# Kernel optimization log

Measured on AMD Instinct MI355X. Metric: run time of the kernel, lower is better.

Reference implementation:

```python
import jax, jax.numpy as jnp
import numpy as np

N, E, HIN, H, FC, C, G = 50000, 1600000, 7, 128, 256, 2, 512

def _glorot(k, shape):
    fan = shape[0] + shape[1]
    return jax.random.uniform(k, shape, jnp.float32, -1.0, 1.0) * jnp.sqrt(6.0 / fan)

def setup_inputs() -> dict:
    key = jax.random.key(0)
    ks = jax.random.split(key, 40)
    inp = {}
    inp['x'] = jax.random.normal(ks[0], (N, HIN), jnp.float32)
    inp['edge_index'] = jax.random.randint(ks[1], (2, E), 0, N)
    inp['batch'] = jnp.sort(jax.random.randint(ks[2], (N,), 0, G))
    dims = [(HIN, H), (H, H), (H, H)]
    for i, (di, do) in enumerate(dims):
        kk = jax.random.split(ks[3 + i], 3)
        inp[f'Wl{i}'] = _glorot(kk[0], (di, do))
        inp[f'bl{i}'] = jnp.zeros((do,), jnp.float32)
        inp[f'Wr{i}'] = _glorot(kk[1], (di, do))
        inp[f'br{i}'] = jnp.zeros((do,), jnp.float32)
        inp[f'att{i}'] = _glorot(kk[2], (1, do))[0]  # GATv2 att vector [H]
        inp[f'bo{i}'] = jnp.zeros((do,), jnp.float32)
    inp['fc1_W'] = _glorot(ks[10], (H, FC))
    inp['fc1_b'] = jnp.zeros((FC,), jnp.float32)
    inp['fc2_W'] = _glorot(ks[11], (FC, C))
    inp['fc2_b'] = jnp.zeros((C,), jnp.float32)
    return inp

def reference(x, edge_index, batch,
              Wl0, bl0, Wr0, br0, att0, bo0,
              Wl1, bl1, Wr1, br1, att1, bo1,
              Wl2, bl2, Wr2, br2, att2, bo2,
              fc1_W, fc1_b, fc2_W, fc2_b):
    n = x.shape[0]
    loop = jnp.arange(n)
    src = jnp.concatenate([edge_index[0], loop])  # self-loops (PyG default)
    dst = jnp.concatenate([edge_index[1], loop])

    def conv(h, Wl, bl, Wr, br, att, bo):
        xl = h @ Wl + bl               # [N,H] source transform
        xr = h @ Wr + br               # [N,H] target transform
        m = jax.nn.leaky_relu(xl[src] + xr[dst], 0.2)  # [E+N,H]
        e = m @ att                    # [E+N] attention logits
        emax = jax.ops.segment_max(e, dst, num_segments=n)
        w = jnp.exp(e - emax[dst])
        denom = jax.ops.segment_sum(w, dst, num_segments=n)
        alpha = w / denom[dst]         # per-target softmax
        return jax.ops.segment_sum(alpha[:, None] * xl[src], dst, num_segments=n) + bo

    h = jax.nn.elu(conv(x, Wl0, bl0, Wr0, br0, att0, bo0))
    h = jax.nn.elu(conv(h, Wl1, bl1, Wr1, br1, att1, bo1))
    h = jax.nn.elu(conv(h, Wl2, bl2, Wr2, br2, att2, bo2))

    # global_mean_pool
    sums = jax.ops.segment_sum(h, batch, num_segments=G)
    cnt = jax.ops.segment_sum(jnp.ones((n,), h.dtype), batch, num_segments=G)
    g = sums / jnp.maximum(cnt, 1.0)[:, None]

    z = jax.nn.relu(g @ fc1_W + fc1_b)
    logits = z @ fc2_W + fc2_b
    return jax.nn.log_softmax(logits, axis=1)
```

## Files before the change

kernel.cpp:

```cpp
#include <hip/hip_runtime.h>
#include <hip/hip_fp16.h>
#include <math.h>

#define H 128
#define FCD 256
#define BUKSH 7
#define MAXBUK 512

typedef _Float16 half8 __attribute__((ext_vector_type(8)));
typedef float floatx4 __attribute__((ext_vector_type(4)));
typedef float fv2 __attribute__((ext_vector_type(2)));

__device__ __forceinline__ fv2 h2fv2(__half2 h){
  float2 t = __half22float2(h);
  fv2 r; r.x = t.x; r.y = t.y; return r;
}

template<int CTRL>
__device__ __forceinline__ float dppadd(float x){
  return x + __int_as_float(__builtin_amdgcn_update_dpp(
      0, __float_as_int(x), CTRL, 0xf, 0xf, true));
}
__device__ __forceinline__ float grp16_sum(float x){
  x = dppadd<0x128>(x);
  x = dppadd<0x124>(x);
  x = dppadd<0x122>(x);
  x = dppadd<0x121>(x);
  return x;
}

__global__ __launch_bounds__(256) void k_setup(
    const float* __restrict__ x,
    const float* __restrict__ Wl0, const float* __restrict__ bl0,
    const float* __restrict__ Wr0, const float* __restrict__ br0,
    __half* __restrict__ xl, __half* __restrict__ xr, int n,
    const float* __restrict__ Wl1, const float* __restrict__ Wr1,
    const float* __restrict__ Wl2, const float* __restrict__ Wr2,
    _Float16* __restrict__ Wt,
    const int* __restrict__ ei, int E, int Et, int* __restrict__ bhistM,
    int NB7, int NEB){
  __shared__ int lh[MAXBUK];
  int b = blockIdx.x, t = threadIdx.x;
  if (b < NB7){
    int col = t & 127;
    int n0 = b*16 + (t >> 7)*8;
    float accl[8], accr[8];
    float bL = bl0[col], bR = br0[col];
    #pragma unroll
    for (int q=0;q<8;q++){ accl[q]=bL; accr[q]=bR; }
    #pragma unroll
    for (int k=0;k<7;k++){
      float wl = Wl0[k*H + col];
      float wr = Wr0[k*H + col];
      #pragma unroll
      for (int q=0;q<8;q++){
        int node = n0+q; if (node >= n) node = n-1;
        float hv = x[(size_t)node*7 + k];
        accl[q] = fmaf(hv, wl, accl[q]);
        accr[q] = fmaf(hv, wr, accr[q]);
      }
    }
    #pragma unroll
    for (int q=0;q<8;q++){
      int node = n0+q;
      if (node < n){
        xl[(size_t)node*H + col] = __float2half(accl[q]);
        xr[(size_t)node*H + col] = __float2half(accr[q]);
      }
    }
  } else if (b < NB7 + 256){
    int idx = (b - NB7)*256 + t;
    int e    = idx & 7;
    int lane = (idx >> 3) & 63;
    int kb   = (idx >> 9) & 3;
    int nt   = (idx >> 11) & 15;
    int L    = idx >> 15;
    int m16 = lane & 15, quad = lane >> 4;
    int k = kb*32 + quad*8 + e;
    int nn = nt*16 + m16;
    const float* W = (L==0) ? (nn<H?Wl1:Wr1) : (nn<H?Wl2:Wr2);
    Wt[idx] = (_Float16)W[k*H + (nn&127)];
  } else {
    int r = b - NB7 - 256;
    lh[t] = 0; lh[t+256] = 0;
    __syncthreads();
    int j0 = r*8192;
    #pragma unroll 4
    for (int i=0;i<32;i++){
      int j = j0 + i*256 + t;
      if (j < Et){
        int dst = (j < E) ? ei[E+j] : (j - E);
        atomicAdd(&lh[dst>>BUKSH], 1);
      }
    }
    __syncthreads();
    bhistM[r*MAXBUK + t]       = lh[t];
    bhistM[r*MAXBUK + 256 + t] = lh[t+256];
  }
}

__global__ void k_scanB(const int* __restrict__ bhistM, int nrows,
                        int* __restrict__ bbase, int* __restrict__ bnext){
  int t = threadIdx.x, lane = t & 63, w = t >> 6;
  int v = 0;
  for (int r=0; r<nrows; r++) v += bhistM[r*MAXBUK + t];
  int x = v;
  #pragma unroll
  for (int off=1; off<64; off<<=1){
    int y = __shfl_up(x, off);
    if (lane >= off) x += y;
  }
  __shared__ int ws[8];
  if (lane==63) ws[w] = x;
  __syncthreads();
  int wo = 0;
  #pragma unroll
  for (int i=0;i<8;i++) if (i<w) wo += ws[i];
  int excl = wo + x - v;
  bbase[t] = excl; bnext[t] = excl;
  if (t==511) bbase[512] = wo + x;
}

__global__ void k_bscatter(const int* __restrict__ ei, int E, int Et, int nbuk,
                           int* __restrict__ bnext, unsigned* __restrict__ ebuf){
  __shared__ int lh[MAXBUK];
  __shared__ int lbase[MAXBUK];
  int t = threadIdx.x;
  lh[t] = 0;
  __syncthreads();
  int j0 = blockIdx.x*8192;
  unsigned pk[16]; int bk[16]; int rk[16];
  #pragma unroll
  for (int i=0;i<16;i++){
    int j = j0 + i*512 + t;
    if (j < Et){
      int src, dst;
      if (j < E){ src = ei[j]; dst = ei[E+j]; } else { src = dst = j - E; }
      pk[i] = (unsigned)src | ((unsigned)dst << 16);
      bk[i] = dst >> BUKSH;
      rk[i] = atomicAdd(&lh[bk[i]], 1);
    }
  }
  __syncthreads();
  if (t < nbuk){
    int c = lh[t];
    lbase[t] = c ? atomicAdd(&bnext[t], c) : 0;
  }
  __syncthreads();
  #pragma unroll
  for (int i=0;i<16;i++){
    int j = j0 + i*512 + t;
    if (j < Et) ebuf[lbase[bk[i]] + rk[i]] = pk[i];
  }
}

__global__ void k_bfill(const unsigned* __restrict__ ebuf, const int* __restrict__ bbase,
                        int N, int Et,
                        int* __restrict__ row_ptr, int* __restrict__ csr,
                        int* __restrict__ perm){
  __shared__ int cnt[1<<BUKSH];
  __shared__ int lnxt[1<<BUKSH];
  __shared__ int bh[256];
  __shared__ int sbase[256];
  __shared__ int rk[256];
  __shared__ int ws0[1];
  __shared__ int ws2[4];
  int b = blockIdx.x, t = threadIdx.x;
  if (t < (1<<BUKSH)) cnt[t] = 0;
  bh[t] = 0; rk[t] = 0;
  if (b==0 && t==0) row_ptr[N] = Et;
  __syncthreads();
  int lo = bbase[b], hi = bbase[b+1];
  for (int j = lo + t; j < hi; j += 256){
    unsigned d = ebuf[j] >> 16;
    atomicAdd(&cnt[d & ((1<<BUKSH)-1)], 1);
  }
  __syncthreads();
  int lane = t & 63;
  int mydeg = (t < (1<<BUKSH)) ? cnt[t] : 0;
  int x = mydeg;
  #pragma unroll
  for (int off=1; off<64; off<<=1){
    int y = __shfl_up(x, off);
    if (lane >= off) x += y;
  }
  if (t==63) ws0[0] = x;
  __syncthreads();
  if (t >= 64 && t < 128) x += ws0[0];
  int node = (b<<BUKSH) + t;
  if (t < (1<<BUKSH)){
    int excl = lo + x - mydeg;
    lnxt[t] = excl;
    if (node < N){
      row_ptr[node] = excl;
      atomicAdd(&bh[min(mydeg,255)], 1);
    }
  }
  __syncthreads();
  for (int j = lo + t; j < hi; j += 256){
    unsigned e = ebuf[j];
    int d = (e >> 16) & ((1<<BUKSH)-1);
    int r = atomicAdd(&lnxt[d], 1);
    csr[r] = (int)((e & 0xffff) << 8);
  }
  int bv = bh[t];
  int bx = bv;
  int w2 = t >> 6;
  #pragma unroll
  for (int off=1; off<64; off<<=1){
    int y = __shfl_up(bx, off);
    if (lane >= off) bx += y;
  }
  if (lane==63) ws2[w2] = bx;
  __syncthreads();
  int wo = (w2>0?ws2[0]:0) + (w2>1?ws2[1]:0) + (w2>2?ws2[2]:0);
  sbase[t] = wo + bx - bv;
  __syncthreads();
  if (t < (1<<BUKSH) && node < N){
    int d = min(mydeg,255);
    int r = atomicAdd(&rk[d], 1);
    perm[(b<<BUKSH) + sbase[d] + r] = node;
  }
}

__global__ __launch_bounds__(256) void k_gemm2h(
    const __half* __restrict__ h, const _Float16* __restrict__ Wt,
    const float* __restrict__ bl, const float* __restrict__ br,
    __half* __restrict__ xl, __half* __restrict__ xr, int n){
  int wave = threadIdx.x >> 6, lane = threadIdx.x & 63;
  int m16 = lane & 15, quad = lane >> 4;
  int row0 = blockIdx.x*64 + wave*16;
  int arow = row0 + m16; if (arow >= n) arow = n-1;
  const __half* hr = h + (size_t)arow*H;
  half8 a[4];
  #pragma unroll
  for (int kb=0;kb<4;kb++) a[kb] = *(const half8*)(hr + kb*32 + quad*8);
  floatx4 acc[16];
  #pragma unroll
  for (int t=0;t<16;t++){ floatx4 z = {0.f,0.f,0.f,0.f}; acc[t] = z; }
  #pragma unroll
  for (int nt=0;nt<16;nt++){
    const _Float16* bp = Wt + ((size_t)nt*4)*512 + lane*8;
    #pragma unroll
    for (int kb=0;kb<4;kb++){
      half8 b = *(const half8*)(bp + kb*512);
      acc[nt] = __builtin_amdgcn_mfma_f32_16x16x32_f16(a[kb], b, acc[nt], 0,0,0);
    }
  }
  #pragma unroll
  for (int nt=0;nt<16;nt++){
    int c = nt*16 + m16;
    float bias; __half* dst; int cc;
    if (c < H){ bias = bl[c];   dst = xl; cc = c;   }
    else      { bias = br[c-H]; dst = xr; cc = c-H; }
    #pragma unroll
    for (int r=0;r<4;r++){
      int rw = row0 + quad*4 + r;
      if (rw < n) dst[(size_t)rw*H + cc] = __float2half(acc[nt][r] + bias);
    }
  }
}

__global__ void k_gat(const __half* __restrict__ xl, const __half* __restrict__ xr,
                      const float* __restrict__ att, const float* __restrict__ bo,
                      const int* __restrict__ row_ptr, const int* __restrict__ csr_src,
                      const int* __restrict__ perm,
                      __half* __restrict__ hout, int n){
  int gid0 = (int)((blockIdx.x*blockDim.x + threadIdx.x) >> 4);
  int lane16 = threadIdx.x & 15;
  if (gid0 >= n) return;
  int gid = perm[n-1-gid0];
  const char* xlb = (const char*)xl + lane16*16;
  int f = lane16*8;
  fv2 xr2[4], a6[4], a4[4];
  {
    union { float4 q; __half2 h[4]; } U;
    U.q = *(const float4*)(xr + (size_t)gid*H + f);
    #pragma unroll
    for (int i=0;i<4;i++) xr2[i] = h2fv2(U.h[i]);
    float4 q0 = *(const float4*)(att + f);
    float4 q1 = *(const float4*)(att + f + 4);
    fv2 av[4];
    av[0].x=q0.x; av[0].y=q0.y; av[1].x=q0.z; av[1].y=q0.w;
    av[2].x=q1.x; av[2].y=q1.y; av[3].x=q1.z; av[3].y=q1.w;
    #pragma unroll
    for (int i=0;i<4;i++){ a6[i] = av[i]*0.6f; a4[i] = av[i]*0.4f; }
  }
  fv2 acc2[4];
  #pragma unroll
  for (int i=0;i<4;i++){ acc2[i].x = 0.f; acc2[i].y = 0.f; }
  float mmax = -INFINITY, denom = 0.f;
  int beg = row_ptr[gid], end = row_ptr[gid+1];
  int j = beg;
  for (; j+7 < end; j += 8){
    int s[8];
    #pragma unroll
    for (int u=0;u<8;u++) s[u] = csr_src[j+u];
    float4 r[8];
    #pragma unroll
    for (int u=0;u<8;u++) r[u] = *(const float4*)(xlb + s[u]);
    float d[8];
    #pragma unroll
    for (int u=0;u<8;u++){
      union { float4 q; __half2 h[4]; } U; U.q = r[u];
      fv2 d2; d2.x = 0.f; d2.y = 0.f;
      #pragma unroll
      for (int i=0;i<4;i++){
        fv2 uu = h2fv2(U.h[i]) + xr2[i];
        d2 += uu * a6[i];
        d2 += __builtin_elementwise_abs(uu) * a4[i];
      }
      d[u] = d2.x + d2.y;
    }
    #pragma unroll
    for (int u=0;u<8;u++) d[u] = grp16_sum(d[u]);
    float m8 = fmaxf(fmaxf(fmaxf(d[0],d[1]), fmaxf(d[2],d[3])),
                     fmaxf(fmaxf(d[4],d[5]), fmaxf(d[6],d[7])));
    if (m8 > mmax){
      float sc = __expf(mmax - m8);
      #pragma unroll
      for (int i=0;i<4;i++) acc2[i] *= sc;
      denom *= sc;
      mmax = m8;
    }
    #pragma unroll
    for (int u=0;u<8;u++){
      float w = __expf(d[u] - mmax);
      denom += w;
      union { float4 q; __half2 h[4]; } U; U.q = r[u];
      #pragma unroll
      for (int i=0;i<4;i++) acc2[i] += h2fv2(U.h[i]) * w;
    }
  }
  for (; j<end; j++){
    int s0 = csr_src[j];
    union { float4 q; __half2 h[4]; } U;
    U.q = *(const float4*)(xlb + s0);
    fv2 v2[4];
    #pragma unroll
    for (int i=0;i<4;i++) v2[i] = h2fv2(U.h[i]);
    fv2 d2; d2.x = 0.f; d2.y = 0.f;
    #pragma unroll
    for (int i=0;i<4;i++){
      fv2 uu = v2[i] + xr2[i];
      d2 += uu * a6[i];
      d2 += __builtin_elementwise_abs(uu) * a4[i];
    }
    float dd = d2.x + d2.y;
    dd = grp16_sum(dd);
    if (dd > mmax){
      float sc = __expf(mmax - dd);
      #pragma unroll
      for (int i=0;i<4;i++) acc2[i] *= sc;
      denom *= sc;
      mmax = dd;
    }
    float w = __expf(dd - mmax);
    denom += w;
    #pragma unroll
    for (int i=0;i<4;i++) acc2[i] += v2[i] * w;
  }
  float inv = 1.f/denom;
  float o[8];
  {
    float4 b0 = *(const float4*)(bo + f);
    float4 b1 = *(const float4*)(bo + f + 4);
    float bb[8] = {b0.x,b0.y,b0.z,b0.w,b1.x,b1.y,b1.z,b1.w};
    #pragma unroll
    for (int i=0;i<4;i++){
      float t0 = acc2[i].x*inv + bb[2*i];
      float t1 = acc2[i].y*inv + bb[2*i+1];
      o[2*i]   = t0 > 0.f ? t0 : expm1f(t0);
      o[2*i+1] = t1 > 0.f ? t1 : expm1f(t1);
    }
  }
  union { float4 f4; __half2 h2[4]; } u;
  #pragma unroll
  for (int i=0;i<4;i++) u.h2[i] = __floats2half2_rn(o[2*i], o[2*i+1]);
  *(float4*)(hout + (size_t)gid*H + f) = u.f4;
}

__global__ void k_fc(const __half* __restrict__ hbuf, const int* __restrict__ batch, int N,
                     const float* __restrict__ W1, const float* __restrict__ b1,
                     const float* __restrict__ W2, const float* __restrict__ b2,
                     float* __restrict__ out){
  __shared__ float g[H];
  __shared__ float2 part[4][64];
  __shared__ float zs[FCD];
  __shared__ int bounds[2];
  int gi = blockIdx.x;
  int t = threadIdx.x;
  if (t < 2){
    int target = gi + t;
    int lo = 0, hi = N;
    while (lo < hi){ int mid = (lo+hi)>>1; if (batch[mid] < target) lo = mid+1; else hi = mid; }
    bounds[t] = lo;
  }
  __syncthreads();
  int lo = bounds[0], hi = bounds[1];
  int pairc = t & 63, slice = t >> 6;
  float sx = 0.f, sy = 0.f;
  for (int node = lo + slice; node < hi; node += 4){
    float2 f2 = __half22float2(*(const __half2*)(hbuf + (size_t)node*H + pairc*2));
    sx += f2.x; sy += f2.y;
  }
  part[slice][pairc] = make_float2(sx, sy);
  __syncthreads();
  if (t < 64){
    float2 a = part[0][t], b = part[1][t], c = part[2][t], d = part[3][t];
    float cnt = (float)(hi - lo); if (cnt < 1.f) cnt = 1.f;
    float inv = 1.f/cnt;
    g[2*t]   = (a.x+b.x+c.x+d.x)*inv;
    g[2*t+1] = (a.y+b.y+c.y+d.y)*inv;
  }
  __syncthreads();
  float acc = b1[t];
  for (int k=0;k<H;k++) acc = fmaf(g[k], W1[k*FCD+t], acc);
  zs[t] = acc > 0.f ? acc : 0.f;
  __syncthreads();
  if (t < 2){
    float l = b2[t];
    for (int k=0;k<FCD;k++) l = fmaf(zs[k], W2[k*2+t], l);
    g[t] = l;
  }
  __syncthreads();
  if (t < 2){
    float l0 = g[0], l1 = g[1];
    float mx = fmaxf(l0,l1);
    float lse = mx + logf(__expf(l0-mx) + __expf(l1-mx));
    out[gi*2+t] = g[t] - lse;
  }
}

extern "C" void kernel_launch(void* const* d_in, const int* in_sizes, int n_in,
                              void* d_out, int out_size, void* d_ws, size_t ws_size,
                              hipStream_t stream) {
  const float* x     = (const float*)d_in[0];
  const int*   ei    = (const int*)  d_in[1];
  const int*   batch = (const int*)  d_in[2];
  const float* Wl[3]  = {(const float*)d_in[3],  (const float*)d_in[9],  (const float*)d_in[15]};
  const float* bl[3]  = {(const float*)d_in[4],  (const float*)d_in[10], (const float*)d_in[16]};
  const float* Wr[3]  = {(const float*)d_in[5],  (const float*)d_in[11], (const float*)d_in[17]};
  const float* br[3]  = {(const float*)d_in[6],  (const float*)d_in[12], (const float*)d_in[18]};
  const float* att[3] = {(const float*)d_in[7],  (const float*)d_in[13], (const float*)d_in[19]};
  const float* bo[3]  = {(const float*)d_in[8],  (const float*)d_in[14], (const float*)d_in[20]};
  const float* fc1W = (const float*)d_in[21];
  const float* fc1b = (const float*)d_in[22];
  const float* fc2W = (const float*)d_in[23];
  const float* fc2b = (const float*)d_in[24];

  const int N  = in_sizes[2];
  const int E  = in_sizes[1]/2;
  const int Et = E + N;
  const int G  = out_size/2;
  const int NBUK = (N + (1<<BUKSH)-1) >> BUKSH;
  const int NEB = (Et + 8191)/8192;
  const int NB7 = (N + 15)/16;

  char* p = (char*)d_ws;
  auto alloc = [&](size_t bytes)->void*{
    void* r = (void*)p; p += (bytes + 255) & ~(size_t)255; return r;
  };
  int*      row_ptr = (int*)     alloc((size_t)(N+1)*4);
  int*      bbase   = (int*)     alloc((size_t)(MAXBUK+8)*4);
  int*      bnext   = (int*)     alloc((size_t)(MAXBUK+8)*4);
  int*      bhistM  = (int*)     alloc((size_t)NEB*MAXBUK*4);
  int*      perm    = (int*)     alloc((size_t)N*4);
  int*      csr     = (int*)     alloc((size_t)Et*4);
  unsigned* ebuf    = (unsigned*)alloc((size_t)Et*4);
  __half*   xl      = (__half*)  alloc((size_t)N*H*2);
  __half*   xr      = (__half*)  alloc((size_t)N*H*2);
  __half*   hbuf    = (__half*)  alloc((size_t)N*H*2);
  _Float16* Wt      = (_Float16*)alloc((size_t)2*16*4*512*2);

  k_setup<<<NB7 + 256 + NEB, 256, 0, stream>>>(
      x, Wl[0], bl[0], Wr[0], br[0], xl, xr, N,
      Wl[1], Wr[1], Wl[2], Wr[2], Wt,
      ei, E, Et, bhistM, NB7, NEB);
  k_scanB<<<1, 512, 0, stream>>>(bhistM, NEB, bbase, bnext);
  k_bscatter<<<NEB, 512, 0, stream>>>(ei, E, Et, NBUK, bnext, ebuf);
  k_bfill<<<NBUK, 256, 0, stream>>>(ebuf, bbase, N, Et, row_ptr, csr, perm);

  const int gM  = (N + 63)/64;
  const int gg  = (int)(((size_t)N*16 + 255)/256);

  k_gat<<<gg, 256, 0, stream>>>(xl, xr, att[0], bo[0], row_ptr, csr, perm, hbuf, N);
  k_gemm2h<<<gM, 256, 0, stream>>>(hbuf, Wt, bl[1], br[1], xl, xr, N);
  k_gat<<<gg, 256, 0, stream>>>(xl, xr, att[1], bo[1], row_ptr, csr, perm, hbuf, N);
  k_gemm2h<<<gM, 256, 0, stream>>>(hbuf, Wt + (size_t)16*4*512, bl[2], br[2], xl, xr, N);
  k_gat<<<gg, 256, 0, stream>>>(xl, xr, att[2], bo[2], row_ptr, csr, perm, hbuf, N);

  k_fc<<<G, 256, 0, stream>>>(hbuf, batch, N, fc1W, fc1b, fc2W, fc2b, (float*)d_out);
}
```

Before: 459.0 us.

## Build global degree-sorted node permutation via two-pass histogram scan

The node permutation was previously sorted by degree only within each 128-node bucket. Now each block stores per-node degrees and a degree histogram, a new scan kernel computes global offsets per degree bin, and a scatter kernel places nodes into a globally degree-sorted order. This should give the GAT kernels better load balance, since nodes of similar degree land in the same wavefronts, at the cost of two extra small kernel launches in preprocessing.

```diff
diff --git a/kernel.cpp b/kernel.cpp
--- a/kernel.cpp
+++ b/kernel.cpp
@@ -156,18 +156,15 @@
 
 __global__ void k_bfill(const unsigned* __restrict__ ebuf, const int* __restrict__ bbase,
                         int N, int Et,
-                        int* __restrict__ row_ptr, int* __restrict__ csr,
-                        int* __restrict__ perm){
+                        int* __restrict__ row_ptr, int* __restrict__ deg,
+                        int* __restrict__ csr, int* __restrict__ histsT){
   __shared__ int cnt[1<<BUKSH];
   __shared__ int lnxt[1<<BUKSH];
   __shared__ int bh[256];
-  __shared__ int sbase[256];
-  __shared__ int rk[256];
   __shared__ int ws0[1];
-  __shared__ int ws2[4];
   int b = blockIdx.x, t = threadIdx.x;
   if (t < (1<<BUKSH)) cnt[t] = 0;
-  bh[t] = 0; rk[t] = 0;
+  bh[t] = 0;
   if (b==0 && t==0) row_ptr[N] = Et;
   __syncthreads();
   int lo = bbase[b], hi = bbase[b+1];
@@ -177,8 +174,8 @@
   }
   __syncthreads();
   int lane = t & 63;
-  int mydeg = (t < (1<<BUKSH)) ? cnt[t] : 0;
-  int x = mydeg;
+  int v = (t < (1<<BUKSH)) ? cnt[t] : 0;
+  int x = v;
   #pragma unroll
   for (int off=1; off<64; off<<=1){
     int y = __shfl_up(x, off);
@@ -187,39 +184,74 @@
   if (t==63) ws0[0] = x;
   __syncthreads();
   if (t >= 64 && t < 128) x += ws0[0];
-  int node = (b<<BUKSH) + t;
   if (t < (1<<BUKSH)){
-    int excl = lo + x - mydeg;
+    int node = (b<<BUKSH) + t;
+    int excl = lo + x - v;
     lnxt[t] = excl;
     if (node < N){
       row_ptr[node] = excl;
-      atomicAdd(&bh[min(mydeg,255)], 1);
-    }
-  }
-  __syncthreads();
+      deg[node] = v;
+      atomicAdd(&bh[min(v,255)], 1);
+    }
+  }
+  __syncthreads();
+  histsT[t*MAXBUK + b] = bh[t];
   for (int j = lo + t; j < hi; j += 256){
     unsigned e = ebuf[j];
     int d = (e >> 16) & ((1<<BUKSH)-1);
     int r = atomicAdd(&lnxt[d], 1);
     csr[r] = (int)((e & 0xffff) << 8);
   }
-  int bv = bh[t];
-  int bx = bv;
-  int w2 = t >> 6;
+}
+
+__global__ void k_dbinscan(int* __restrict__ histsT, int nb, int* __restrict__ bintot){
+  int d = blockIdx.x;
+  int t = threadIdx.x, lane = t & 63, w = t >> 6;
+  int v = (t<nb) ? histsT[d*MAXBUK + t] : 0;
+  int x = v;
   #pragma unroll
   for (int off=1; off<64; off<<=1){
-    int y = __shfl_up(bx, off);
-    if (lane >= off) bx += y;
-  }
-  if (lane==63) ws2[w2] = bx;
-  __syncthreads();
-  int wo = (w2>0?ws2[0]:0) + (w2>1?ws2[1]:0) + (w2>2?ws2[2]:0);
-  sbase[t] = wo + bx - bv;
-  __syncthreads();
-  if (t < (1<<BUKSH) && node < N){
-    int d = min(mydeg,255);
-    int r = atomicAdd(&rk[d], 1);
-    perm[(b<<BUKSH) + sbase[d] + r] = node;
+    int y = __shfl_up(x, off);
+    if (lane >= off) x += y;
+  }
+  __shared__ int ws[8];
+  if (lane==63) ws[w] = x;
+  __syncthreads();
+  int wo = 0;
+  #pragma unroll
+  for (int i=0;i<8;i++) if (i<w) wo += ws[i];
+  if (t<nb) histsT[d*MAXBUK + t] = wo + x - v;
+  if (t==511) bintot[d] = wo + x;
+}
+
+__global__ void k_dscatter2(const int* __restrict__ deg, int N,
+                            const int* __restrict__ histsT, const int* __restrict__ bintot,
+                            int* __restrict__ perm){
+  __shared__ int lh[256];
+  __shared__ int sbase[256];
+  __shared__ int ws[4];
+  int t = threadIdx.x, b = blockIdx.x;
+  int lane = t & 63, w = t >> 6;
+  int v = bintot[t];
+  int x = v;
+  #pragma unroll
+  for (int off=1; off<64; off<<=1){
+    int y = __shfl_up(x, off);
+    if (lane >= off) x += y;
+  }
+  if (lane==63) ws[w] = x;
+  lh[t] = 0;
+  __syncthreads();
+  int wo = (w>0?ws[0]:0) + (w>1?ws[1]:0) + (w>2?ws[2]:0);
+  sbase[t] = wo + x - v;
+  __syncthreads();
+  if (t < 128){
+    int i = (b<<BUKSH) + t;
+    if (i < N){
+      int d = min(deg[i],255);
+      int r = atomicAdd(&lh[d], 1);
+      perm[sbase[d] + histsT[d*MAXBUK + b] + r] = i;
+    }
   }
 }
 
@@ -461,10 +493,13 @@
   auto alloc = [&](size_t bytes)->void*{
     void* r = (void*)p; p += (bytes + 255) & ~(size_t)255; return r;
   };
+  int*      deg     = (int*)     alloc((size_t)N*4);
   int*      row_ptr = (int*)     alloc((size_t)(N+1)*4);
   int*      bbase   = (int*)     alloc((size_t)(MAXBUK+8)*4);
   int*      bnext   = (int*)     alloc((size_t)(MAXBUK+8)*4);
   int*      bhistM  = (int*)     alloc((size_t)NEB*MAXBUK*4);
+  int*      histsT  = (int*)     alloc((size_t)256*MAXBUK*4);
+  int*      bintot  = (int*)     alloc((size_t)260*4);
   int*      perm    = (int*)     alloc((size_t)N*4);
   int*      csr     = (int*)     alloc((size_t)Et*4);
   unsigned* ebuf    = (unsigned*)alloc((size_t)Et*4);
@@ -479,7 +514,9 @@
       ei, E, Et, bhistM, NB7, NEB);
   k_scanB<<<1, 512, 0, stream>>>(bhistM, NEB, bbase, bnext);
   k_bscatter<<<NEB, 512, 0, stream>>>(ei, E, Et, NBUK, bnext, ebuf);
-  k_bfill<<<NBUK, 256, 0, stream>>>(ebuf, bbase, N, Et, row_ptr, csr, perm);
+  k_bfill<<<NBUK, 256, 0, stream>>>(ebuf, bbase, N, Et, row_ptr, deg, csr, histsT);
+  k_dbinscan<<<256, 512, 0, stream>>>(histsT, NBUK, bintot);
+  k_dscatter2<<<NBUK, 256, 0, stream>>>(deg, N, histsT, bintot, perm);
 
   const int gM  = (N + 63)/64;
   const int gg  = (int)(((size_t)N*16 + 255)/256);
```

After: 438.4 us. 1.05x faster.
